# Optimization experiments

Measured on AMD Instinct MI355X. Metric: run time of the kernel, lower is better.

Reference implementation:

```python
import jax, jax.numpy as jnp
import numpy as np

B, S, T, D, V = 512, 128, 128, 512, 128  # batch, enc len, dec steps (=longest_smi), dim_model, output_size


def setup_inputs() -> dict:
    key = jax.random.key(0)
    ks = jax.random.split(key, 17)
    sc = 0.05
    return {
        "e_all": jax.random.normal(ks[0], (B, S, D), jnp.float32),
        "e_h": jax.random.normal(ks[1], (1, B, D), jnp.float32),
        "e_c": jax.random.normal(ks[2], (1, B, D), jnp.float32),
        "target": jax.random.randint(ks[3], (B, T), 0, T),
        # params (Linear weights stored [in, out], y = x @ W + b)
        "E": jax.random.normal(ks[4], (T, D), jnp.float32) * sc,        # Embedding(longest_smi, D)
        "Wa": jax.random.normal(ks[5], (D, D), jnp.float32) * sc,
        "ba": jnp.zeros((D,), jnp.float32),
        "Ua": jax.random.normal(ks[6], (D, D), jnp.float32) * sc,
        "bu": jnp.zeros((D,), jnp.float32),
        "Va": jax.random.normal(ks[7], (D, 1), jnp.float32) * sc,
        "bv": jnp.zeros((1,), jnp.float32),
        "W_ih": jax.random.normal(ks[8], (2 * D, 4 * D), jnp.float32) * sc,
        "b_ih": jnp.zeros((4 * D,), jnp.float32),
        "W_hh": jax.random.normal(ks[9], (D, 4 * D), jnp.float32) * sc,
        "b_hh": jnp.zeros((4 * D,), jnp.float32),
        "W_out": jax.random.normal(ks[10], (D, V), jnp.float32) * sc,
        "b_out": jnp.zeros((V,), jnp.float32),
    }


def reference(e_all, e_h, e_c, target, E, Wa, ba, Ua, bu, Va, bv,
              W_ih, b_ih, W_hh, b_hh, W_out, b_out):
    Bb = e_all.shape[0]
    # teacher forcing: step 0 input is token 0 (SOS), then target[:, :-1]
    idx = jnp.concatenate([jnp.zeros((Bb, 1), target.dtype), target[:, :-1]], axis=1)  # [B,T]
    emb_all = E[idx]                       # [B,T,D] (dropout is identity in eval)
    keys_proj = e_all @ Ua + bu            # Ua(keys), loop-invariant  [B,S,D]
    h0, c0 = e_h[0], e_c[0]                # [B,D]

    def step(carry, emb):
        h, c = carry
        q = (h + c) @ Wa + ba                                   # [B,D]  Wa(query)
        s = jnp.tanh(q[:, None, :] + keys_proj) @ Va + bv       # [B,S,1]
        w = jax.nn.softmax(s[..., 0], axis=-1)                  # [B,S]
        ctx = jnp.einsum('bs,bsd->bd', w, e_all)                # [B,D]
        x = jnp.concatenate([emb, ctx], axis=-1)                # [B,2D]
        g = x @ W_ih + b_ih + h @ W_hh + b_hh                   # [B,4D], torch gate order i,f,g,o
        i_, f_, g_, o_ = jnp.split(g, 4, axis=-1)
        c2 = jax.nn.sigmoid(f_) * c + jax.nn.sigmoid(i_) * jnp.tanh(g_)
        h2 = jax.nn.sigmoid(o_) * jnp.tanh(c2)
        out = h2 @ W_out + b_out                                # [B,V]
        return (h2, c2), (out, w)

    _, (outs, attns) = jax.lax.scan(step, (h0, c0), jnp.swapaxes(emb_all, 0, 1))
    outputs = jax.nn.log_softmax(jnp.swapaxes(outs, 0, 1), axis=-1)  # [B,T,V]
    cross_attn = jnp.swapaxes(attns, 0, 1)                           # [B,T,S]
    return outputs, cross_attn
```

## Files before the change

kernel.cpp:

```cpp
#include <hip/hip_runtime.h>

#define B_ 512
#define S_ 128
#define T_ 128
#define D_ 512
#define V_ 128
#define LDW 72

typedef __attribute__((ext_vector_type(8))) short s16x8;
typedef __attribute__((ext_vector_type(4))) short s16x4;
typedef __attribute__((ext_vector_type(4))) float f32x4;

__device__ __forceinline__ float b2f(unsigned short h) {
    union { unsigned int u; float f; } x; x.u = ((unsigned int)h) << 16; return x.f;
}
__device__ __forceinline__ unsigned short f2b(float f) {
    union { float f; unsigned int u; } x; x.f = f;
    unsigned int u = x.u; u += 0x7FFFu + ((u >> 16) & 1u);
    return (unsigned short)(u >> 16);
}
#if __has_builtin(__builtin_amdgcn_rcpf)
__device__ __forceinline__ float rcp_f(float x) { return __builtin_amdgcn_rcpf(x); }
#else
__device__ __forceinline__ float rcp_f(float x) { return 1.0f / x; }
#endif
__device__ __forceinline__ float sigm(float x) { return rcp_f(1.0f + __expf(-x)); }
__device__ __forceinline__ float tanh_fast(float x) {
    float e = __expf(2.0f * fabsf(x));
    float r = 1.0f - 2.0f * rcp_f(e + 1.0f);
    return copysignf(r, x);
}

struct P {
    const int* target;
    const float* E; const float* bv; const float* ba; const float* bout;
    const short* vab;
    const short* ealb; const short* kpb;
    const short* WaT; const short* WehT; const short* WctxT; const short* WoutT;
    const float* bcat;
    short* qbf; short* xeh; short* ctxb; float* gp;
    short* hcbf; short* h2bf; float* cst;
    float* out_logits; float* out_attn;
};

struct AttnS { float scp[4][64]; float wbuf[S_]; float cpart[4][D_]; };
struct PG128 { short As[128][LDW]; short Bs[128][LDW]; };
struct OutS  { short As[64][LDW]; short Bs[128][LDW]; };
union SharedA { AttnS a; PG128 g; OutS o; };

__device__ __forceinline__ void attn_phase(const P& p, AttnS& sh, int b, int step)
{
    const int t = threadIdx.x, lane = t & 63, wave = t >> 6;
    {
        const int sg = wave & 1, dh = wave >> 1;
        const int s = sg * 64 + lane;
        const short* kr = p.kpb + ((size_t)b * S_ + s) * D_ + dh * 256;
        const short* qv = p.qbf + (size_t)b * D_ + dh * 256;
        const short* vv = p.vab + dh * 256;
        float acc = 0.f;
        #pragma unroll 4
        for (int i = 0; i < 32; ++i) {
            s16x8 kv = *(const s16x8*)(kr + i * 8);
            s16x8 qk = *(const s16x8*)(qv + i * 8);
            s16x8 vk = *(const s16x8*)(vv + i * 8);
            #pragma unroll
            for (int j = 0; j < 8; ++j)
                acc += tanh_fast(b2f((unsigned short)qk[j]) + b2f((unsigned short)kv[j]))
                       * b2f((unsigned short)vk[j]);
        }
        sh.scp[wave][lane] = acc;
    }
    __syncthreads();
    if (wave == 0) {
        const float bvv = p.bv[0];
        float v0 = sh.scp[0][lane] + sh.scp[2][lane] + bvv;
        float v1 = sh.scp[1][lane] + sh.scp[3][lane] + bvv;
        float m = fmaxf(v0, v1);
        #pragma unroll
        for (int o = 32; o >= 1; o >>= 1) m = fmaxf(m, __shfl_xor(m, o));
        float e0 = __expf(v0 - m), e1 = __expf(v1 - m);
        float su = e0 + e1;
        #pragma unroll
        for (int o = 32; o >= 1; o >>= 1) su += __shfl_xor(su, o);
        float inv = rcp_f(su);
        float w0 = e0 * inv, w1 = e1 * inv;
        sh.wbuf[lane] = w0; sh.wbuf[lane + 64] = w1;
        float* ao = p.out_attn + ((size_t)b * T_ + step) * S_;
        ao[lane] = w0; ao[lane + 64] = w1;
    }
    __syncthreads();
    {
        const int d0 = lane * 8;
        f32x4 aA = {0.f,0.f,0.f,0.f}, aB = {0.f,0.f,0.f,0.f};
        const short* eb = p.ealb + (size_t)b * S_ * D_ + d0;
        #pragma unroll 4
        for (int i = 0; i < 32; ++i) {
            int s = wave * 32 + i;
            float wv = sh.wbuf[s];
            s16x8 ev = *(const s16x8*)(eb + (size_t)s * D_);
            #pragma unroll
            for (int j = 0; j < 4; ++j) aA[j] += wv * b2f((unsigned short)ev[j]);
            #pragma unroll
            for (int j = 0; j < 4; ++j) aB[j] += wv * b2f((unsigned short)ev[4 + j]);
        }
        *(f32x4*)&sh.cpart[wave][d0]     = aA;
        *(f32x4*)&sh.cpart[wave][d0 + 4] = aB;
    }
    __syncthreads();
    {
        int dd = t * 2;
        float v0 = sh.cpart[0][dd]   + sh.cpart[1][dd]   + sh.cpart[2][dd]   + sh.cpart[3][dd];
        float v1 = sh.cpart[0][dd+1] + sh.cpart[1][dd+1] + sh.cpart[2][dd+1] + sh.cpart[3][dd+1];
        short2 o2; o2.x = (short)f2b(v0); o2.y = (short)f2b(v1);
        *(short2*)(p.ctxb + (size_t)b * D_ + dd) = o2;
    }
}

__device__ __forceinline__ void pgate_phase(const P& p, PG128& sh, int bid2)
{
    const int t = threadIdx.x, lane = t & 63, wave = t >> 6;
    const int wr = wave >> 1, wc = wave & 1;
    const int lrow = lane & 15, kq = lane >> 4;
    const int m0 = (bid2 >> 4) * 128, n0 = (bid2 & 15) * 128;
    const int K = 1024;
    f32x4 acc[4][4] = {};
    for (int k0 = 0; k0 < K; k0 += 64) {
        s16x8 va[4], vb[4];
        #pragma unroll
        for (int r = 0; r < 4; ++r) {
            int idx = r * 256 + t, row = idx >> 3, seg = idx & 7;
            va[r] = *(const s16x8*)(p.xeh  + (size_t)(m0 + row) * K + k0 + seg * 8);
            vb[r] = *(const s16x8*)(p.WehT + (size_t)(n0 + row) * K + k0 + seg * 8);
        }
        __syncthreads();
        #pragma unroll
        for (int r = 0; r < 4; ++r) {
            int idx = r * 256 + t, row = idx >> 3, seg = idx & 7;
            *(s16x8*)(&sh.As[row][seg * 8]) = va[r];
            *(s16x8*)(&sh.Bs[row][seg * 8]) = vb[r];
        }
        __syncthreads();
        #pragma unroll
        for (int kk = 0; kk < 64; kk += 32) {
            s16x8 af[4], bf[4];
            #pragma unroll
            for (int f = 0; f < 4; ++f) {
                af[f] = *(const s16x8*)(&sh.As[wr * 64 + f * 16 + lrow][kk + kq * 8]);
                bf[f] = *(const s16x8*)(&sh.Bs[wc * 64 + f * 16 + lrow][kk + kq * 8]);
            }
            #pragma unroll
            for (int fa = 0; fa < 4; ++fa)
                #pragma unroll
                for (int fb = 0; fb < 4; ++fb)
                    acc[fa][fb] = __builtin_amdgcn_mfma_f32_16x16x32_bf16(af[fa], bf[fb], acc[fa][fb], 0, 0, 0);
        }
    }
    #pragma unroll
    for (int fa = 0; fa < 4; ++fa)
        #pragma unroll
        for (int fb = 0; fb < 4; ++fb) {
            int col = n0 + wc * 64 + fb * 16 + lrow;
            float bvv = p.bcat[col];
            #pragma unroll
            for (int j = 0; j < 4; ++j) {
                int row = m0 + wr * 64 + fa * 16 + kq * 4 + j;
                p.gp[(size_t)row * 2048 + col] = acc[fa][fb][j] + bvv;
            }
        }
}

struct GateS { short As[64][LDW]; short Bs[64][LDW]; float gt[64][65]; };

__device__ __forceinline__ void fgate_phase(const P& p, GateS& sh, int bid, int step)
{
    const int t = threadIdx.x, lane = t & 63, wave = t >> 6;
    const int wr = wave >> 1, wc = wave & 1;
    const int lrow = lane & 15, kq = lane >> 4;
    const int srow = t >> 3, sseg = t & 7;
    const int m0 = (bid >> 5) * 64, n0 = (bid & 31) * 64;
    f32x4 acc[2][2] = {};
    for (int k0 = 0; k0 < 512; k0 += 64) {
        s16x8 va0 = *(const s16x8*)(p.ctxb + (size_t)(m0 + srow) * 512 + k0 + sseg * 8);
        s16x8 va1 = *(const s16x8*)(p.ctxb + (size_t)(m0 + srow + 32) * 512 + k0 + sseg * 8);
        s16x8 vb0 = *(const s16x8*)(p.WctxT + (size_t)(n0 + srow) * 512 + k0 + sseg * 8);
        s16x8 vb1 = *(const s16x8*)(p.WctxT + (size_t)(n0 + srow + 32) * 512 + k0 + sseg * 8);
        __syncthreads();
        *(s16x8*)(&sh.As[srow][sseg * 8]) = va0;
        *(s16x8*)(&sh.As[srow + 32][sseg * 8]) = va1;
        *(s16x8*)(&sh.Bs[srow][sseg * 8]) = vb0;
        *(s16x8*)(&sh.Bs[srow + 32][sseg * 8]) = vb1;
        __syncthreads();
        #pragma unroll
        for (int kk = 0; kk < 64; kk += 32) {
            s16x8 af0 = *(const s16x8*)(&sh.As[wr * 32 + lrow][kk + kq * 8]);
            s16x8 af1 = *(const s16x8*)(&sh.As[wr * 32 + 16 + lrow][kk + kq * 8]);
            s16x8 bf0 = *(const s16x8*)(&sh.Bs[wc * 32 + lrow][kk + kq * 8]);
            s16x8 bf1 = *(const s16x8*)(&sh.Bs[wc * 32 + 16 + lrow][kk + kq * 8]);
            acc[0][0] = __builtin_amdgcn_mfma_f32_16x16x32_bf16(af0, bf0, acc[0][0], 0, 0, 0);
            acc[0][1] = __builtin_amdgcn_mfma_f32_16x16x32_bf16(af0, bf1, acc[0][1], 0, 0, 0);
            acc[1][0] = __builtin_amdgcn_mfma_f32_16x16x32_bf16(af1, bf0, acc[1][0], 0, 0, 0);
            acc[1][1] = __builtin_amdgcn_mfma_f32_16x16x32_bf16(af1, bf1, acc[1][1], 0, 0, 0);
        }
    }
    #pragma unroll
    for (int m2 = 0; m2 < 2; ++m2)
        #pragma unroll
        for (int n2 = 0; n2 < 2; ++n2) {
            int cl = wc * 32 + n2 * 16 + lrow;
            #pragma unroll
            for (int j = 0; j < 4; ++j) {
                int rl = wr * 32 + m2 * 16 + kq * 4 + j;
                sh.gt[rl][cl] = acc[m2][n2][j] + p.gp[(size_t)(m0 + rl) * 2048 + n0 + cl];
            }
        }
    __syncthreads();
    const int rl4 = t >> 4, dl = t & 15;
    #pragma unroll
    for (int pass = 0; pass < 4; ++pass) {
        int row = pass * 16 + rl4;
        int b = m0 + row;
        int d = (n0 >> 2) + dl;
        float gi = sh.gt[row][dl * 4 + 0];
        float gf = sh.gt[row][dl * 4 + 1];
        float gg = sh.gt[row][dl * 4 + 2];
        float go = sh.gt[row][dl * 4 + 3];
        float cv = p.cst[(size_t)b * D_ + d];
        float c2 = sigm(gf) * cv + sigm(gi) * tanh_fast(gg);
        float h2 = sigm(go) * tanh_fast(c2);
        p.cst[(size_t)b * D_ + d] = c2;
        p.hcbf[(size_t)b * D_ + d] = (short)f2b(h2 + c2);
        p.h2bf[(size_t)b * D_ + d] = (short)f2b(h2);
        p.xeh[(size_t)b * 1024 + 512 + d] = (short)f2b(h2);
        int tok = p.target[b * T_ + step];
        p.xeh[(size_t)b * 1024 + d] = (short)f2b(p.E[(size_t)tok * D_ + d]);
    }
}

__device__ __forceinline__ void q_phase(const P& p, OutS& sh, int bid)
{
    const int t = threadIdx.x, lane = t & 63, wave = t >> 6;
    const int lrow = lane & 15, kq = lane >> 4;
    const int srow = t >> 3, sseg = t & 7;
    const int m0 = (bid >> 4) * 64, n0 = (bid & 15) * 32;
    f32x4 acc0 = {}, acc1 = {};
    for (int k0 = 0; k0 < 512; k0 += 64) {
        s16x8 va0 = *(const s16x8*)(p.hcbf + (size_t)(m0 + srow) * 512 + k0 + sseg * 8);
        s16x8 va1 = *(const s16x8*)(p.hcbf + (size_t)(m0 + srow + 32) * 512 + k0 + sseg * 8);
        s16x8 vb0 = *(const s16x8*)(p.WaT + (size_t)(n0 + srow) * 512 + k0 + sseg * 8);
        __syncthreads();
        *(s16x8*)(&sh.As[srow][sseg * 8]) = va0;
        *(s16x8*)(&sh.As[srow + 32][sseg * 8]) = va1;
        if (srow < 32) *(s16x8*)(&sh.Bs[srow][sseg * 8]) = vb0;
        __syncthreads();
        #pragma unroll
        for (int kk = 0; kk < 64; kk += 32) {
            s16x8 af  = *(const s16x8*)(&sh.As[wave * 16 + lrow][kk + kq * 8]);
            s16x8 bf0 = *(const s16x8*)(&sh.Bs[lrow][kk + kq * 8]);
            s16x8 bf1 = *(const s16x8*)(&sh.Bs[16 + lrow][kk + kq * 8]);
            acc0 = __builtin_amdgcn_mfma_f32_16x16x32_bf16(af, bf0, acc0, 0, 0, 0);
            acc1 = __builtin_amdgcn_mfma_f32_16x16x32_bf16(af, bf1, acc1, 0, 0, 0);
        }
    }
    #pragma unroll
    for (int n2 = 0; n2 < 2; ++n2) {
        int col = n0 + n2 * 16 + lrow;
        float bvv = p.ba[col];
        f32x4 av = n2 ? acc1 : acc0;
        #pragma unroll
        for (int j = 0; j < 4; ++j) {
            int row = m0 + wave * 16 + kq * 4 + j;
            p.qbf[(size_t)row * 512 + col] = (short)f2b(av[j] + bvv);
        }
    }
}

__device__ __forceinline__ void out_phase(const P& p, OutS& sh, int obid, int step)
{
    const int t = threadIdx.x, lane = t & 63, wave = t >> 6;
    const int lrow = lane & 15, kq = lane >> 4;
    const int srow = t >> 3, sseg = t & 7;
    const int m0 = obid * 64;
    f32x4 acc[8] = {};
    for (int k0 = 0; k0 < 512; k0 += 64) {
        s16x8 va0 = *(const s16x8*)(p.h2bf + (size_t)(m0 + srow) * 512 + k0 + sseg * 8);
        s16x8 va1 = *(const s16x8*)(p.h2bf + (size_t)(m0 + srow + 32) * 512 + k0 + sseg * 8);
        s16x8 vb[4];
        #pragma unroll
        for (int p4 = 0; p4 < 4; ++p4)
            vb[p4] = *(const s16x8*)(p.WoutT + (size_t)(srow + p4 * 32) * 512 + k0 + sseg * 8);
        __syncthreads();
        *(s16x8*)(&sh.As[srow][sseg * 8]) = va0;
        *(s16x8*)(&sh.As[srow + 32][sseg * 8]) = va1;
        #pragma unroll
        for (int p4 = 0; p4 < 4; ++p4) *(s16x8*)(&sh.Bs[srow + p4 * 32][sseg * 8]) = vb[p4];
        __syncthreads();
        #pragma unroll
        for (int kk = 0; kk < 64; kk += 32) {
            s16x8 a = *(const s16x8*)(&sh.As[wave * 16 + lrow][kk + kq * 8]);
            #pragma unroll
            for (int f = 0; f < 8; ++f) {
                s16x8 b = *(const s16x8*)(&sh.Bs[f * 16 + lrow][kk + kq * 8]);
                acc[f] = __builtin_amdgcn_mfma_f32_16x16x32_bf16(a, b, acc[f], 0, 0, 0);
            }
        }
    }
    float colb[8];
    #pragma unroll
    for (int f = 0; f < 8; ++f) colb[f] = p.bout[f * 16 + lrow];
    #pragma unroll
    for (int j = 0; j < 4; ++j) {
        float v[8]; float mx = -1e30f;
        #pragma unroll
        for (int f = 0; f < 8; ++f) { v[f] = acc[f][j] + colb[f]; mx = fmaxf(mx, v[f]); }
        #pragma unroll
        for (int o = 1; o < 16; o <<= 1) mx = fmaxf(mx, __shfl_xor(mx, o));
        float sum = 0.f;
        #pragma unroll
        for (int f = 0; f < 8; ++f) sum += __expf(v[f] - mx);
        #pragma unroll
        for (int o = 1; o < 16; o <<= 1) sum += __shfl_xor(sum, o);
        float lse = mx + __logf(sum);
        int row = m0 + wave * 16 + kq * 4 + j;
        float* orow = p.out_logits + ((size_t)row * T_ + step) * V_;
        #pragma unroll
        for (int f = 0; f < 8; ++f) orow[f * 16 + lrow] = v[f] - lse;
    }
}

__global__ __launch_bounds__(256, 2) void kA(P p, int step) {
    __shared__ SharedA sh;
    const int bid = blockIdx.x;
    if (bid < 512)       attn_phase(p, sh.a, bid, step);
    else if (bid < 576)  pgate_phase(p, sh.g, bid - 512);
    else if (step > 0)   out_phase(p, sh.o, bid - 576, step - 1);
}
__global__ __launch_bounds__(256, 2) void kB(P p, int step) {
    __shared__ GateS sh;
    fgate_phase(p, sh, blockIdx.x, step);
}
__global__ __launch_bounds__(256, 2) void kC(P p) {
    __shared__ OutS sh;
    q_phase(p, sh, blockIdx.x);
}
__global__ __launch_bounds__(256, 2) void kOutLast(P p, int step) {
    __shared__ OutS sh;
    out_phase(p, sh, blockIdx.x, step);
}

template<bool OUT_BF16>
__global__ __launch_bounds__(256)
void gemm64(const short* __restrict__ A, const short* __restrict__ Bt,
            const float* __restrict__ bias, void* __restrict__ Cp,
            int M, int N, int K)
{
    __shared__ __align__(16) short As[64][LDW];
    __shared__ __align__(16) short Bs[64][LDW];
    const int t = threadIdx.x;
    const int lane = t & 63, wave = t >> 6;
    const int wr = wave >> 1, wc = wave & 1;
    const int lrow = lane & 15, kq = lane >> 4;
    const int m0 = blockIdx.y * 64, n0 = blockIdx.x * 64;
    const int srow = t >> 3, sseg = t & 7;
    f32x4 acc[2][2] = {};
    for (int k0 = 0; k0 < K; k0 += 64) {
        s16x8 va0 = *(const s16x8*)(A + (size_t)(m0 + srow) * K + k0 + sseg * 8);
        s16x8 va1 = *(const s16x8*)(A + (size_t)(m0 + srow + 32) * K + k0 + sseg * 8);
        s16x8 vb0 = *(const s16x8*)(Bt + (size_t)(n0 + srow) * K + k0 + sseg * 8);
        s16x8 vb1 = *(const s16x8*)(Bt + (size_t)(n0 + srow + 32) * K + k0 + sseg * 8);
        __syncthreads();
        *(s16x8*)(&As[srow][sseg * 8]) = va0;
        *(s16x8*)(&As[srow + 32][sseg * 8]) = va1;
        *(s16x8*)(&Bs[srow][sseg * 8]) = vb0;
        *(s16x8*)(&Bs[srow + 32][sseg * 8]) = vb1;
        __syncthreads();
        for (int kk = 0; kk < 64; kk += 32) {
            s16x8 af[2], bf[2];
            af[0] = *(const s16x8*)(&As[wr * 32 + lrow][kk + kq * 8]);
            af[1] = *(const s16x8*)(&As[wr * 32 + 16 + lrow][kk + kq * 8]);
            bf[0] = *(const s16x8*)(&Bs[wc * 32 + lrow][kk + kq * 8]);
            bf[1] = *(const s16x8*)(&Bs[wc * 32 + 16 + lrow][kk + kq * 8]);
            for (int m2 = 0; m2 < 2; ++m2)
                for (int n2 = 0; n2 < 2; ++n2)
                    acc[m2][n2] = __builtin_amdgcn_mfma_f32_16x16x32_bf16(af[m2], bf[n2], acc[m2][n2], 0, 0, 0);
        }
    }
    for (int m2 = 0; m2 < 2; ++m2)
        for (int n2 = 0; n2 < 2; ++n2) {
            int col = n0 + wc * 32 + n2 * 16 + lrow;
            float bvv = bias ? bias[col] : 0.0f;
            for (int j = 0; j < 4; ++j) {
                int row = m0 + wr * 32 + m2 * 16 + kq * 4 + j;
                float v = acc[m2][n2][j] + bvv;
                if (OUT_BF16) ((short*)Cp)[(size_t)row * N + col] = (short)f2b(v);
                else          ((float*)Cp)[(size_t)row * N + col] = v;
            }
        }
}

__global__ __launch_bounds__(256)
void init_state(const float* __restrict__ e_h, const float* __restrict__ e_c,
                float* __restrict__ c, short* __restrict__ hcbf,
                short* __restrict__ xeh, const float* __restrict__ E)
{
    int gid = blockIdx.x * 256 + threadIdx.x;
    int b = gid >> 9, d = gid & 511;
    float h0 = e_h[gid], c0 = e_c[gid];
    c[gid] = c0;
    hcbf[gid] = (short)f2b(h0 + c0);
    xeh[(size_t)b * 1024 + 512 + d] = (short)f2b(h0);
    xeh[(size_t)b * 1024 + d] = (short)f2b(E[d]);
}

__global__ __launch_bounds__(256)
void transpose_cast(const float* __restrict__ in, short* __restrict__ out,
                    int N, int ostride, int koff, int gate_perm)
{
    __shared__ float tile[64][65];
    int t = threadIdx.x;
    int n0 = blockIdx.x * 64, k0 = blockIdx.y * 64;
    int cc = t & 63, r4 = t >> 6;
    for (int i = 0; i < 16; ++i) {
        int r = i * 4 + r4;
        tile[r][cc] = in[(size_t)(k0 + r) * N + n0 + cc];
    }
    __syncthreads();
    for (int i = 0; i < 16; ++i) {
        int nr = i * 4 + r4;
        int ng = n0 + nr;
        int np = gate_perm ? ((ng & 511) * 4 + (ng >> 9)) : ng;
        out[(size_t)np * ostride + koff + k0 + cc] = (short)f2b(tile[cc][nr]);
    }
}

__global__ __launch_bounds__(256)
void cast_bf16_v4(const float* __restrict__ in, short* __restrict__ out, int n4)
{
    int i = blockIdx.x * 256 + threadIdx.x;
    int stride = gridDim.x * 256;
    for (; i < n4; i += stride) {
        f32x4 v = ((const f32x4*)in)[i];
        s16x4 o;
        for (int j = 0; j < 4; ++j) o[j] = (short)f2b(v[j]);
        ((s16x4*)out)[i] = o;
    }
}

__global__ __launch_bounds__(256)
void make_bcat(const float* __restrict__ b_ih, const float* __restrict__ b_hh, float* __restrict__ bcat)
{
    int i = blockIdx.x * 256 + threadIdx.x;
    if (i < 2048) {
        int np = (i & 511) * 4 + (i >> 9);
        bcat[np] = b_ih[i] + b_hh[i];
    }
}

extern "C" void kernel_launch(void* const* d_in, const int* in_sizes, int n_in,
                              void* d_out, int out_size, void* d_ws, size_t ws_size,
                              hipStream_t stream)
{
    const float* e_all  = (const float*)d_in[0];
    const float* e_h    = (const float*)d_in[1];
    const float* e_c    = (const float*)d_in[2];
    const int*   target = (const int*)d_in[3];
    const float* E      = (const float*)d_in[4];
    const float* Wa     = (const float*)d_in[5];
    const float* ba     = (const float*)d_in[6];
    const float* Ua     = (const float*)d_in[7];
    const float* bu     = (const float*)d_in[8];
    const float* Va     = (const float*)d_in[9];
    const float* bv     = (const float*)d_in[10];
    const float* W_ih   = (const float*)d_in[11];
    const float* b_ih   = (const float*)d_in[12];
    const float* W_hh   = (const float*)d_in[13];
    const float* b_hh   = (const float*)d_in[14];
    const float* W_out  = (const float*)d_in[15];
    const float* b_out  = (const float*)d_in[16];

    char* ws = (char*)d_ws;
    size_t off = 0;
    auto alloc = [&](size_t bytes) { void* p = ws + off; off += (bytes + 255) & ~255ull; return p; };
    short* ealb  = (short*)alloc((size_t)B_ * S_ * D_ * 2);
    short* kpb   = (short*)alloc((size_t)B_ * S_ * D_ * 2);
    short* WaT   = (short*)alloc((size_t)D_ * D_ * 2);
    short* UaT   = (short*)alloc((size_t)D_ * D_ * 2);
    short* WehT  = (short*)alloc((size_t)2048 * 1024 * 2);
    short* WctxT = (short*)alloc((size_t)2048 * 512 * 2);
    short* WoutT = (short*)alloc((size_t)V_ * D_ * 2);
    float* bcat  = (float*)alloc(2048 * 4);
    short* qbf   = (short*)alloc((size_t)B_ * D_ * 2);
    short* vab   = (short*)alloc((size_t)D_ * 2);
    short* xeh   = (short*)alloc((size_t)B_ * 1024 * 2);
    short* ctxb  = (short*)alloc((size_t)B_ * D_ * 2);
    float* gp    = (float*)alloc((size_t)B_ * 2048 * 4);
    short* hcbf  = (short*)alloc((size_t)B_ * D_ * 2);
    short* h2bf  = (short*)alloc((size_t)B_ * D_ * 2);
    float* cst   = (float*)alloc((size_t)B_ * D_ * 4);
    if (off > ws_size) return;

    float* out_logits = (float*)d_out;
    float* out_attn   = (float*)d_out + (size_t)B_ * T_ * V_;

    cast_bf16_v4<<<4096, 256, 0, stream>>>(e_all, ealb, B_ * S_ * D_ / 4);
    cast_bf16_v4<<<1,    256, 0, stream>>>(Va, vab, D_ / 4);
    transpose_cast<<<dim3(8, 8),  256, 0, stream>>>(Wa,  WaT,  512,  512, 0, 0);
    transpose_cast<<<dim3(8, 8),  256, 0, stream>>>(Ua,  UaT,  512,  512, 0, 0);
    transpose_cast<<<dim3(32, 8), 256, 0, stream>>>(W_ih,              WehT,  2048, 1024, 0,   1);
    transpose_cast<<<dim3(32, 8), 256, 0, stream>>>(W_ih + 512 * 2048, WctxT, 2048, 512,  0,   1);
    transpose_cast<<<dim3(32, 8), 256, 0, stream>>>(W_hh,              WehT,  2048, 1024, 512, 1);
    transpose_cast<<<dim3(2, 8),  256, 0, stream>>>(W_out, WoutT, 128, 512, 0, 0);
    make_bcat<<<8, 256, 0, stream>>>(b_ih, b_hh, bcat);
    gemm64<true><<<dim3(8, 1024), 256, 0, stream>>>(ealb, UaT, bu, kpb, B_ * S_, 512, 512);
    init_state<<<1024, 256, 0, stream>>>(e_h, e_c, cst, hcbf, xeh, E);
    gemm64<true><<<dim3(8, 8), 256, 0, stream>>>(hcbf, WaT, ba, qbf, B_, 512, 512);

    P pp;
    pp.target = target; pp.E = E; pp.bv = bv; pp.ba = ba; pp.bout = b_out;
    pp.vab = vab;
    pp.ealb = ealb; pp.kpb = kpb; pp.WaT = WaT; pp.WehT = WehT; pp.WctxT = WctxT; pp.WoutT = WoutT;
    pp.bcat = bcat; pp.qbf = qbf; pp.xeh = xeh; pp.ctxb = ctxb; pp.gp = gp;
    pp.hcbf = hcbf; pp.h2bf = h2bf; pp.cst = cst;
    pp.out_logits = out_logits; pp.out_attn = out_attn;

    for (int t = 0; t < T_; ++t) {
        kA<<<584, 256, 0, stream>>>(pp, t);
        kB<<<256, 256, 0, stream>>>(pp, t);
        if (t < T_ - 1) kC<<<128, 256, 0, stream>>>(pp);
    }
    kOutLast<<<8, 256, 0, stream>>>(pp, T_ - 1);
    (void)n_in; (void)in_sizes; (void)out_size;
}
```

Before: 7.442 ms.

## Move pre-gate GEMM and output projection into the q-projection kernel

The [x_emb, h] @ [W_ih_emb; W_hh] pre-gate GEMM and the output projection move out of the attention kernel and into kC, which now also computes the next query projection. The pre-gate GEMM is retiled from 64 blocks of 128x128 to 128 blocks of 128x64, so more CUs share that work. The initial query GEMM and the separate final-output kernel are replaced by an INIT variant of kC and a kC launch on every step. The attention kernel now has only 512 uniform blocks, so heterogeneous blocks no longer sit on its critical path. In exchange, kC does more work per launch, and the final step runs q and pgate work that nothing uses.

```diff
diff --git a/kernel.cpp b/kernel.cpp
--- a/kernel.cpp
+++ b/kernel.cpp
@@ -44,9 +44,10 @@
 };
 
 struct AttnS { float scp[4][64]; float wbuf[S_]; float cpart[4][D_]; };
-struct PG128 { short As[128][LDW]; short Bs[128][LDW]; };
 struct OutS  { short As[64][LDW]; short Bs[128][LDW]; };
-union SharedA { AttnS a; PG128 g; OutS o; };
+struct PG2   { short As[128][LDW]; short Bs[64][LDW]; };
+struct GateS { short As[64][LDW]; short Bs[64][LDW]; float gt[64][65]; };
+union SharedC { OutS o; PG2 g; };
 
 __device__ __forceinline__ void attn_phase(const P& p, AttnS& sh, int b, int step)
 {
@@ -116,20 +117,23 @@
     }
 }
 
-__device__ __forceinline__ void pgate_phase(const P& p, PG128& sh, int bid2)
+__device__ __forceinline__ void pgate_phase(const P& p, PG2& sh, int bid2)
 {
     const int t = threadIdx.x, lane = t & 63, wave = t >> 6;
-    const int wr = wave >> 1, wc = wave & 1;
     const int lrow = lane & 15, kq = lane >> 4;
-    const int m0 = (bid2 >> 4) * 128, n0 = (bid2 & 15) * 128;
+    const int m0 = (bid2 >> 5) * 128, n0 = (bid2 & 31) * 64;
     const int K = 1024;
-    f32x4 acc[4][4] = {};
+    f32x4 acc[2][4] = {};
     for (int k0 = 0; k0 < K; k0 += 64) {
-        s16x8 va[4], vb[4];
+        s16x8 va[4], vb[2];
         #pragma unroll
         for (int r = 0; r < 4; ++r) {
             int idx = r * 256 + t, row = idx >> 3, seg = idx & 7;
-            va[r] = *(const s16x8*)(p.xeh  + (size_t)(m0 + row) * K + k0 + seg * 8);
+            va[r] = *(const s16x8*)(p.xeh + (size_t)(m0 + row) * K + k0 + seg * 8);
+        }
+        #pragma unroll
+        for (int r = 0; r < 2; ++r) {
+            int idx = r * 256 + t, row = idx >> 3, seg = idx & 7;
             vb[r] = *(const s16x8*)(p.WehT + (size_t)(n0 + row) * K + k0 + seg * 8);
         }
         __syncthreads();
@@ -137,39 +141,41 @@
         for (int r = 0; r < 4; ++r) {
             int idx = r * 256 + t, row = idx >> 3, seg = idx & 7;
             *(s16x8*)(&sh.As[row][seg * 8]) = va[r];
+        }
+        #pragma unroll
+        for (int r = 0; r < 2; ++r) {
+            int idx = r * 256 + t, row = idx >> 3, seg = idx & 7;
             *(s16x8*)(&sh.Bs[row][seg * 8]) = vb[r];
         }
         __syncthreads();
         #pragma unroll
         for (int kk = 0; kk < 64; kk += 32) {
-            s16x8 af[4], bf[4];
-            #pragma unroll
-            for (int f = 0; f < 4; ++f) {
-                af[f] = *(const s16x8*)(&sh.As[wr * 64 + f * 16 + lrow][kk + kq * 8]);
-                bf[f] = *(const s16x8*)(&sh.Bs[wc * 64 + f * 16 + lrow][kk + kq * 8]);
+            s16x8 af[2], bf[4];
+            af[0] = *(const s16x8*)(&sh.As[wave * 32 + lrow][kk + kq * 8]);
+            af[1] = *(const s16x8*)(&sh.As[wave * 32 + 16 + lrow][kk + kq * 8]);
+            #pragma unroll
+            for (int f = 0; f < 4; ++f)
+                bf[f] = *(const s16x8*)(&sh.Bs[f * 16 + lrow][kk + kq * 8]);
+            #pragma unroll
+            for (int m2 = 0; m2 < 2; ++m2)
+                #pragma unroll
+                for (int n2 = 0; n2 < 4; ++n2)
+                    acc[m2][n2] = __builtin_amdgcn_mfma_f32_16x16x32_bf16(af[m2], bf[n2], acc[m2][n2], 0, 0, 0);
+        }
+    }
+    #pragma unroll
+    for (int m2 = 0; m2 < 2; ++m2)
+        #pragma unroll
+        for (int n2 = 0; n2 < 4; ++n2) {
+            int col = n0 + n2 * 16 + lrow;
+            float bvv = p.bcat[col];
+            #pragma unroll
+            for (int j = 0; j < 4; ++j) {
+                int row = m0 + wave * 32 + m2 * 16 + kq * 4 + j;
+                p.gp[(size_t)row * 2048 + col] = acc[m2][n2][j] + bvv;
             }
-            #pragma unroll
-            for (int fa = 0; fa < 4; ++fa)
-                #pragma unroll
-                for (int fb = 0; fb < 4; ++fb)
-                    acc[fa][fb] = __builtin_amdgcn_mfma_f32_16x16x32_bf16(af[fa], bf[fb], acc[fa][fb], 0, 0, 0);
-        }
-    }
-    #pragma unroll
-    for (int fa = 0; fa < 4; ++fa)
-        #pragma unroll
-        for (int fb = 0; fb < 4; ++fb) {
-            int col = n0 + wc * 64 + fb * 16 + lrow;
-            float bvv = p.bcat[col];
-            #pragma unroll
-            for (int j = 0; j < 4; ++j) {
-                int row = m0 + wr * 64 + fa * 16 + kq * 4 + j;
-                p.gp[(size_t)row * 2048 + col] = acc[fa][fb][j] + bvv;
-            }
-        }
-}
-
-struct GateS { short As[64][LDW]; short Bs[64][LDW]; float gt[64][65]; };
+        }
+}
 
 __device__ __forceinline__ void fgate_phase(const P& p, GateS& sh, int bid, int step)
 {
@@ -246,7 +252,8 @@
     for (int k0 = 0; k0 < 512; k0 += 64) {
         s16x8 va0 = *(const s16x8*)(p.hcbf + (size_t)(m0 + srow) * 512 + k0 + sseg * 8);
         s16x8 va1 = *(const s16x8*)(p.hcbf + (size_t)(m0 + srow + 32) * 512 + k0 + sseg * 8);
-        s16x8 vb0 = *(const s16x8*)(p.WaT + (size_t)(n0 + srow) * 512 + k0 + sseg * 8);
+        int brow = n0 + (srow & 31);
+        s16x8 vb0 = *(const s16x8*)(p.WaT + (size_t)brow * 512 + k0 + sseg * 8);
         __syncthreads();
         *(s16x8*)(&sh.As[srow][sseg * 8]) = va0;
         *(s16x8*)(&sh.As[srow + 32][sseg * 8]) = va1;
@@ -328,29 +335,25 @@
 }
 
 __global__ __launch_bounds__(256, 2) void kA(P p, int step) {
-    __shared__ SharedA sh;
-    const int bid = blockIdx.x;
-    if (bid < 512)       attn_phase(p, sh.a, bid, step);
-    else if (bid < 576)  pgate_phase(p, sh.g, bid - 512);
-    else if (step > 0)   out_phase(p, sh.o, bid - 576, step - 1);
+    __shared__ AttnS sh;
+    attn_phase(p, sh, blockIdx.x, step);
 }
 __global__ __launch_bounds__(256, 2) void kB(P p, int step) {
     __shared__ GateS sh;
     fgate_phase(p, sh, blockIdx.x, step);
 }
-__global__ __launch_bounds__(256, 2) void kC(P p) {
-    __shared__ OutS sh;
-    q_phase(p, sh, blockIdx.x);
-}
-__global__ __launch_bounds__(256, 2) void kOutLast(P p, int step) {
-    __shared__ OutS sh;
-    out_phase(p, sh, blockIdx.x, step);
-}
-
-template<bool OUT_BF16>
+template<bool INIT>
+__global__ __launch_bounds__(256, 2) void kC(P p, int step) {
+    __shared__ SharedC sh;
+    const int bid = blockIdx.x;
+    if (bid < 128)       q_phase(p, sh.o, bid);
+    else if (bid < 256)  pgate_phase(p, sh.g, bid - 128);
+    else if (!INIT)      out_phase(p, sh.o, bid - 256, step);
+}
+
 __global__ __launch_bounds__(256)
 void gemm64(const short* __restrict__ A, const short* __restrict__ Bt,
-            const float* __restrict__ bias, void* __restrict__ Cp,
+            const float* __restrict__ bias, short* __restrict__ Cp,
             int M, int N, int K)
 {
     __shared__ __align__(16) short As[64][LDW];
@@ -390,9 +393,7 @@
             float bvv = bias ? bias[col] : 0.0f;
             for (int j = 0; j < 4; ++j) {
                 int row = m0 + wr * 32 + m2 * 16 + kq * 4 + j;
-                float v = acc[m2][n2][j] + bvv;
-                if (OUT_BF16) ((short*)Cp)[(size_t)row * N + col] = (short)f2b(v);
-                else          ((float*)Cp)[(size_t)row * N + col] = v;
+                Cp[(size_t)row * N + col] = (short)f2b(acc[m2][n2][j] + bvv);
             }
         }
 }
@@ -510,9 +511,8 @@
     transpose_cast<<<dim3(32, 8), 256, 0, stream>>>(W_hh,              WehT,  2048, 1024, 512, 1);
     transpose_cast<<<dim3(2, 8),  256, 0, stream>>>(W_out, WoutT, 128, 512, 0, 0);
     make_bcat<<<8, 256, 0, stream>>>(b_ih, b_hh, bcat);
-    gemm64<true><<<dim3(8, 1024), 256, 0, stream>>>(ealb, UaT, bu, kpb, B_ * S_, 512, 512);
+    gemm64<<<dim3(8, 1024), 256, 0, stream>>>(ealb, UaT, bu, kpb, B_ * S_, 512, 512);
     init_state<<<1024, 256, 0, stream>>>(e_h, e_c, cst, hcbf, xeh, E);
-    gemm64<true><<<dim3(8, 8), 256, 0, stream>>>(hcbf, WaT, ba, qbf, B_, 512, 512);
 
     P pp;
     pp.target = target; pp.E = E; pp.bv = bv; pp.ba = ba; pp.bout = b_out;
@@ -522,11 +522,12 @@
     pp.hcbf = hcbf; pp.h2bf = h2bf; pp.cst = cst;
     pp.out_logits = out_logits; pp.out_attn = out_attn;
 
+    kC<true><<<256, 256, 0, stream>>>(pp, 0);
+
     for (int t = 0; t < T_; ++t) {
-        kA<<<584, 256, 0, stream>>>(pp, t);
+        kA<<<512, 256, 0, stream>>>(pp, t);
         kB<<<256, 256, 0, stream>>>(pp, t);
-        if (t < T_ - 1) kC<<<128, 256, 0, stream>>>(pp);
-    }
-    kOutLast<<<8, 256, 0, stream>>>(pp, T_ - 1);
+        kC<false><<<264, 256, 0, stream>>>(pp, t);
+    }
     (void)n_in; (void)in_sizes; (void)out_size;
 }
```

After: 6.631 ms. -10.9%, faster.
